# Performance work log

Measured on AMD Instinct MI355X. Metric: run time of the kernel, lower is better.

Reference implementation:

```python
import jax, jax.numpy as jnp
import numpy as np

# FIR kernel from resample_kernel=(1,3,3,1): outer product, normalized (gain=1)
_FIR_1D = np.array([1.0, 3.0, 3.0, 1.0], dtype=np.float32)
_FIR = np.outer(_FIR_1D, _FIR_1D)
_FIR = _FIR / _FIR.sum()  # 4x4


def setup_inputs() -> dict:
    key = jax.random.key(0)
    k1, k2, k3 = jax.random.split(key, 3)
    x = jax.random.normal(k1, (16, 256, 64, 64), dtype=jnp.float32)
    # fan_avg uniform init (default_init): variance = 1/fan_avg, fan_in=fan_out=256*9
    scale = float(np.sqrt(3.0 / (256 * 9)))
    w = jax.random.uniform(k2, (256, 256, 3, 3), dtype=jnp.float32, minval=-scale, maxval=scale)
    b = jax.random.normal(k3, (256,), dtype=jnp.float32) * 0.01
    return {"x": x, "w": w, "b": b}


def reference(x, w, b):
    # conv_downsample_2d: upfirdn2d(x, k, pad=(2,2)) then conv2d stride 2, then + bias
    B, C, H, W = x.shape
    # upfirdn2d with up=1, down=1 == zero-padded true convolution with k.
    # k is symmetric so flip is a no-op, but keep it for faithfulness.
    fir = jnp.asarray(_FIR[::-1, ::-1])                       # [4,4]
    fir_k = jnp.tile(fir[None, None, :, :], (C, 1, 1, 1))     # [C,1,4,4] depthwise
    x = jax.lax.conv_general_dilated(
        x, fir_k,
        window_strides=(1, 1),
        padding=((2, 2), (2, 2)),                             # (p+1)//2, p//2 with p=4
        feature_group_count=C,
        dimension_numbers=("NCHW", "OIHW", "NCHW"),
    )                                                          # [B,C,H+1,W+1]
    y = jax.lax.conv_general_dilated(
        x, w,
        window_strides=(2, 2),
        padding="VALID",
        dimension_numbers=("NCHW", "OIHW", "NCHW"),
    )                                                          # [B,outC,H//2,W//2]
    return y + b[None, :, None, None]
```

## Files before the change

### kernel.cpp

```cpp
#include <hip/hip_runtime.h>
#include <hip/hip_bf16.h>

typedef __attribute__((ext_vector_type(8))) short bf16x8;
typedef __attribute__((ext_vector_type(4))) float f32x4;
typedef __attribute__((ext_vector_type(8))) unsigned short u16x8;

#define KD 2304
#define OUT_PER_B (256 * 1024)

static __device__ __forceinline__ ushort f2bf(float f) {
  union { float f; unsigned int i; } v; v.f = f;
  unsigned int x = v.i;
  x += 0x7fffu + ((x >> 16) & 1u);
  return (ushort)(x >> 16);
}
static __device__ __forceinline__ float bf2f(ushort u) {
  union { unsigned int i; float f; } v; v.i = ((unsigned)u) << 16; return v.f;
}

#define GLDS16(gp, lp)                                                         \
  __builtin_amdgcn_global_load_lds(                                            \
      (const __attribute__((address_space(1))) void*)(gp),                     \
      (__attribute__((address_space(3))) void*)(lp), 16, 0, 0)

#define SWZ(g, r) (((g) & 8) | (((g) ^ (r)) & 7))

__global__ __launch_bounds__(256) void k_fir3(const float* __restrict__ x,
                                              ushort* __restrict__ xft,
                                              const float* __restrict__ wsrc,
                                              ushort* __restrict__ wb) {
  __shared__ float sx[32 * 84];
  __shared__ ushort ring[4 * 65 * 34];
  const int band = blockIdx.x;
  const int c0 = blockIdx.y * 32;
  const int b = blockIdx.z;
  const int r0 = band * 13;
  const int t = threadIdx.x;

  {
    int flat = band + 5 * (blockIdx.y + 8 * b);
    for (int iw = flat * 256 + t; iw < 589824; iw += 163840) {
      float v = wsrc[iw];
      int j = iw % 9;
      int t2 = iw / 9;
      int ic = t2 & 255, oc = t2 >> 8;
      wb[oc * KD + j * 256 + ic] = f2bf(v);
    }
  }

  if (t < 128) {
    int r = t >> 2, cs = t & 3;
    sx[r * 84 + (cs < 2 ? 2 + cs : 66 + cs)] = 0.f;
  }

  for (int it = 0; it < 17; ++it) {
    const int ir = r0 - 2 + it;

    float4 rg[2];
    if (it <= 15) {
      if (ir >= 0 && ir < 64) {
#pragma unroll
        for (int i = 0; i < 2; ++i) {
          int f4 = i * 256 + t;
          int c = f4 >> 4, q = f4 & 15;
          rg[i] = *(const float4*)(x +
                    ((size_t)((b * 256 + c0 + c) * 64 + ir) << 6) + q * 4);
        }
      } else {
        rg[0] = rg[1] = make_float4(0.f, 0.f, 0.f, 0.f);
      }
    }

    if (it >= 4) {
      const int o = r0 - 4 + it;
      for (int idx = t; idx < 260; idx += 256) {
        int w = idx >> 2, a = idx & 3;
        u16x8 r4[4];
#pragma unroll
        for (int d = 0; d < 4; ++d) {
          int slot = (o - 2 + d) & 3;
          r4[d] = *(const u16x8*)&ring[(slot * 65 + w) * 34 + a * 8];
        }
        u16x8 ov;
#pragma unroll
        for (int k = 0; k < 8; ++k) {
          float f0 = bf2f(r4[0][k]), f1 = bf2f(r4[1][k]);
          float f2 = bf2f(r4[2][k]), f3 = bf2f(r4[3][k]);
          ov[k] = f2bf(((f0 + f3) + 3.f * (f1 + f2)) * 0.015625f);
        }
        *(u16x8*)&xft[((size_t)(b * 4225 + o * 65 + w) << 8) + c0 + a * 8] = ov;
      }
    }

    if (it <= 15) {
#pragma unroll
      for (int i = 0; i < 2; ++i) {
        int f4 = i * 256 + t;
        int c = f4 >> 4, q = f4 & 15;
        *(float4*)&sx[c * 84 + 4 + q * 4] = rg[i];
      }
    }
    __syncthreads();

    if (it <= 15) {
      ushort* rw = ring + (ir & 3) * 65 * 34;
      for (int idx = t; idx < 544; idx += 256) {
        int g = idx >> 5, c = idx & 31;
        const float* s = &sx[c * 84 + g * 4];
        float4 a0 = *(const float4*)(s);
        float4 a1 = *(const float4*)(s + 4);
        float4 a2 = *(const float4*)(s + 8);
        int w0 = g * 4;
        rw[w0 * 34 + c] = f2bf((a0.z + a1.y) + 3.f * (a0.w + a1.x));
        if (w0 + 1 < 65) rw[(w0 + 1) * 34 + c] = f2bf((a0.w + a1.z) + 3.f * (a1.x + a1.y));
        if (w0 + 2 < 65) rw[(w0 + 2) * 34 + c] = f2bf((a1.x + a1.w) + 3.f * (a1.y + a1.z));
        if (w0 + 3 < 65) rw[(w0 + 3) * 34 + c] = f2bf((a1.y + a2.x) + 3.f * (a1.z + a1.w));
      }
    }
    __syncthreads();
  }
}

__global__ __launch_bounds__(256) void k_gemm3(const ushort* __restrict__ Wb,
                                               const ushort* __restrict__ Xt,
                                               const float* __restrict__ bias,
                                               float* __restrict__ out) {
  __shared__ ushort lA[128 * 128];
  __shared__ ushort lB[64 * 128];
  const int bid = blockIdx.x;
  const int work = (bid & 7) * 64 + (bid >> 3);
  const int ntile = work >> 1;
  const int mtile = work & 1;
  const int m0 = mtile * 128;
  const int n0 = ntile * 64;
  const int t = threadIdx.x;
  const int wid = t >> 6, lane = t & 63;
  const int wm = wid >> 1, wn = wid & 1;
  const int lrow = lane & 15, kgrp = lane >> 4;

  const ushort* aB[8];
#pragma unroll
  for (int i = 0; i < 8; ++i) {
    int idx = i * 256 + t;
    int row = idx >> 4, gL = idx & 15;
    aB[i] = Wb + (size_t)(m0 + row) * KD + SWZ(gL, row) * 8;
  }
  const ushort* bB[4];
#pragma unroll
  for (int i = 0; i < 4; ++i) {
    int idx = i * 256 + t;
    int row = idx >> 4, gL = idx & 15;
    int n = n0 + row;
    int b = n >> 10, oh = (n >> 5) & 31, ow = n & 31;
    bB[i] = Xt + ((size_t)((b * 65 + 2 * oh) * 65 + 2 * ow) << 8) +
            SWZ(gL, row) * 8;
  }

  f32x4 acc[4][2];
#pragma unroll
  for (int i = 0; i < 4; ++i)
#pragma unroll
    for (int j = 0; j < 2; ++j) acc[i][j] = (f32x4){0.f, 0.f, 0.f, 0.f};

  for (int kt = 0; kt < 18; ++kt) {
    const int j = kt >> 1;
    const int dh = j / 3, dw = j - 3 * dh;
    const int boff = (dh * 65 + dw) * 256 + ((kt & 1) << 7);
    const int k0 = kt << 7;
    __syncthreads();
#pragma unroll
    for (int i = 0; i < 8; ++i)
      GLDS16(aB[i] + k0, &lA[(i * 256 + t) * 8]);
#pragma unroll
    for (int i = 0; i < 4; ++i)
      GLDS16(bB[i] + boff, &lB[(i * 256 + t) * 8]);
    __syncthreads();

#pragma unroll
    for (int s = 0; s < 4; ++s) {
      bf16x8 Af[4], Bf[2];
#pragma unroll
      for (int f = 0; f < 4; ++f) {
        int row = wm * 64 + f * 16 + lrow;
        Af[f] = *(const bf16x8*)&lA[row * 128 + SWZ(s * 4 + kgrp, row) * 8];
      }
#pragma unroll
      for (int f = 0; f < 2; ++f) {
        int row = wn * 32 + f * 16 + lrow;
        Bf[f] = *(const bf16x8*)&lB[row * 128 + SWZ(s * 4 + kgrp, row) * 8];
      }
#pragma unroll
      for (int fm = 0; fm < 4; ++fm)
#pragma unroll
        for (int fn = 0; fn < 2; ++fn)
          acc[fm][fn] = __builtin_amdgcn_mfma_f32_16x16x32_bf16(
              Af[fm], Bf[fn], acc[fm][fn], 0, 0, 0);
    }
  }

  f32x4 bv[4];
#pragma unroll
  for (int fm = 0; fm < 4; ++fm)
    bv[fm] = *(const f32x4*)(bias + m0 + wm * 64 + fm * 16 + kgrp * 4);

#pragma unroll
  for (int fm = 0; fm < 4; ++fm) {
#pragma unroll
    for (int fn = 0; fn < 2; ++fn) {
      int nn = n0 + wn * 32 + fn * 16 + lrow;
      int oc = m0 + wm * 64 + fm * 16 + kgrp * 4;
      float* op = out + (size_t)(nn >> 10) * OUT_PER_B + (nn & 1023) +
                  (size_t)oc * 1024;
      op[0]    = acc[fm][fn][0] + bv[fm][0];
      op[1024] = acc[fm][fn][1] + bv[fm][1];
      op[2048] = acc[fm][fn][2] + bv[fm][2];
      op[3072] = acc[fm][fn][3] + bv[fm][3];
    }
  }
}

extern "C" void kernel_launch(void* const* d_in, const int* in_sizes, int n_in,
                              void* d_out, int out_size, void* d_ws, size_t ws_size,
                              hipStream_t stream) {
  const float* x    = (const float*)d_in[0];
  const float* w    = (const float*)d_in[1];
  const float* bias = (const float*)d_in[2];
  float* out = (float*)d_out;

  char* ws = (char*)d_ws;
  ushort* xft = (ushort*)ws;
  ushort* wb  = (ushort*)(ws + 34611200);

  k_fir3<<<dim3(5, 8, 16), 256, 0, stream>>>(x, xft, w, wb);
  k_gemm3<<<512, 256, 0, stream>>>(wb, xft, bias, out);
}
```

Baseline: 68.15 us.

## Split FIR block into independent per-wave channel groups with wave barriers

The FIR prepass now gives each of the four waves its own 8-channel slice with private LDS staging and ring buffers, replacing block-wide __syncthreads with wave-level barriers. This removes the cross-wave synchronization stalls in the 17-iteration row loop and lets waves progress independently. In exchange the vertical pass uses 65 of 64 lanes unevenly (one lane does two columns), and the xft writes become 16-byte chunks per wave rather than coalesced 64-byte groups. Correctness relies on wave-synchronous LDS visibility within a wavefront.

```diff
diff --git a/kernel.cpp b/kernel.cpp
--- a/kernel.cpp
+++ b/kernel.cpp
@@ -25,20 +25,24 @@
 
 #define SWZ(g, r) (((g) & 8) | (((g) ^ (r)) & 7))
 
-__global__ __launch_bounds__(256) void k_fir3(const float* __restrict__ x,
+__global__ __launch_bounds__(256) void k_fir4(const float* __restrict__ x,
                                               ushort* __restrict__ xft,
                                               const float* __restrict__ wsrc,
                                               ushort* __restrict__ wb) {
-  __shared__ float sx[32 * 84];
-  __shared__ ushort ring[4 * 65 * 34];
+  __shared__ float sxAll[4][8 * 84];
+  __shared__ ushort ringAll[4][4 * 65 * 8];
   const int band = blockIdx.x;
-  const int c0 = blockIdx.y * 32;
+  const int cg = blockIdx.y;
   const int b = blockIdx.z;
+  const int t = threadIdx.x;
+  const int wid = t >> 6, lane = t & 63;
+  const int coct = cg * 32 + wid * 8;
   const int r0 = band * 13;
-  const int t = threadIdx.x;
+  float* sx = sxAll[wid];
+  ushort* ring = ringAll[wid];
 
   {
-    int flat = band + 5 * (blockIdx.y + 8 * b);
+    int flat = band + 5 * (cg + 8 * b);
     for (int iw = flat * 256 + t; iw < 589824; iw += 163840) {
       float v = wsrc[iw];
       int j = iw % 9;
@@ -48,38 +52,36 @@
     }
   }
 
-  if (t < 128) {
-    int r = t >> 2, cs = t & 3;
+  if (lane < 32) {
+    int r = lane >> 2, cs = lane & 3;
     sx[r * 84 + (cs < 2 ? 2 + cs : 66 + cs)] = 0.f;
   }
 
   for (int it = 0; it < 17; ++it) {
     const int ir = r0 - 2 + it;
 
-    float4 rg[2];
+    float4 rg0, rg1;
     if (it <= 15) {
       if (ir >= 0 && ir < 64) {
-#pragma unroll
-        for (int i = 0; i < 2; ++i) {
-          int f4 = i * 256 + t;
-          int c = f4 >> 4, q = f4 & 15;
-          rg[i] = *(const float4*)(x +
-                    ((size_t)((b * 256 + c0 + c) * 64 + ir) << 6) + q * 4);
-        }
+        rg0 = *(const float4*)(x +
+              ((size_t)((b * 256 + coct + (lane >> 4)) * 64 + ir) << 6) +
+              (lane & 15) * 4);
+        rg1 = *(const float4*)(x +
+              ((size_t)((b * 256 + coct + 4 + (lane >> 4)) * 64 + ir) << 6) +
+              (lane & 15) * 4);
       } else {
-        rg[0] = rg[1] = make_float4(0.f, 0.f, 0.f, 0.f);
+        rg0 = rg1 = make_float4(0.f, 0.f, 0.f, 0.f);
       }
     }
 
     if (it >= 4) {
       const int o = r0 - 4 + it;
-      for (int idx = t; idx < 260; idx += 256) {
-        int w = idx >> 2, a = idx & 3;
+      for (int w = lane; w < 65; w += 64) {
         u16x8 r4[4];
 #pragma unroll
         for (int d = 0; d < 4; ++d) {
           int slot = (o - 2 + d) & 3;
-          r4[d] = *(const u16x8*)&ring[(slot * 65 + w) * 34 + a * 8];
+          r4[d] = *(const u16x8*)&ring[(slot * 65 + w) * 8];
         }
         u16x8 ov;
 #pragma unroll
@@ -88,36 +90,32 @@
           float f2 = bf2f(r4[2][k]), f3 = bf2f(r4[3][k]);
           ov[k] = f2bf(((f0 + f3) + 3.f * (f1 + f2)) * 0.015625f);
         }
-        *(u16x8*)&xft[((size_t)(b * 4225 + o * 65 + w) << 8) + c0 + a * 8] = ov;
+        *(u16x8*)&xft[((size_t)(b * 4225 + o * 65 + w) << 8) + coct] = ov;
       }
     }
 
     if (it <= 15) {
-#pragma unroll
-      for (int i = 0; i < 2; ++i) {
-        int f4 = i * 256 + t;
-        int c = f4 >> 4, q = f4 & 15;
-        *(float4*)&sx[c * 84 + 4 + q * 4] = rg[i];
-      }
-    }
-    __syncthreads();
+      *(float4*)&sx[(lane >> 4) * 84 + 4 + (lane & 15) * 4] = rg0;
+      *(float4*)&sx[(4 + (lane >> 4)) * 84 + 4 + (lane & 15) * 4] = rg1;
+    }
+    __builtin_amdgcn_wave_barrier();
 
     if (it <= 15) {
-      ushort* rw = ring + (ir & 3) * 65 * 34;
-      for (int idx = t; idx < 544; idx += 256) {
-        int g = idx >> 5, c = idx & 31;
+      ushort* rw = ring + (ir & 3) * 65 * 8;
+      for (int idx = lane; idx < 136; idx += 64) {
+        int g = idx >> 3, c = idx & 7;
         const float* s = &sx[c * 84 + g * 4];
         float4 a0 = *(const float4*)(s);
         float4 a1 = *(const float4*)(s + 4);
         float4 a2 = *(const float4*)(s + 8);
         int w0 = g * 4;
-        rw[w0 * 34 + c] = f2bf((a0.z + a1.y) + 3.f * (a0.w + a1.x));
-        if (w0 + 1 < 65) rw[(w0 + 1) * 34 + c] = f2bf((a0.w + a1.z) + 3.f * (a1.x + a1.y));
-        if (w0 + 2 < 65) rw[(w0 + 2) * 34 + c] = f2bf((a1.x + a1.w) + 3.f * (a1.y + a1.z));
-        if (w0 + 3 < 65) rw[(w0 + 3) * 34 + c] = f2bf((a1.y + a2.x) + 3.f * (a1.z + a1.w));
-      }
-    }
-    __syncthreads();
+        rw[w0 * 8 + c] = f2bf((a0.z + a1.y) + 3.f * (a0.w + a1.x));
+        if (w0 + 1 < 65) rw[(w0 + 1) * 8 + c] = f2bf((a0.w + a1.z) + 3.f * (a1.x + a1.y));
+        if (w0 + 2 < 65) rw[(w0 + 2) * 8 + c] = f2bf((a1.x + a1.w) + 3.f * (a1.y + a1.z));
+        if (w0 + 3 < 65) rw[(w0 + 3) * 8 + c] = f2bf((a1.y + a2.x) + 3.f * (a1.z + a1.w));
+      }
+    }
+    __builtin_amdgcn_wave_barrier();
   }
 }
 
@@ -231,6 +229,6 @@
   ushort* xft = (ushort*)ws;
   ushort* wb  = (ushort*)(ws + 34611200);
 
-  k_fir3<<<dim3(5, 8, 16), 256, 0, stream>>>(x, xft, w, wb);
+  k_fir4<<<dim3(5, 8, 16), 256, 0, stream>>>(x, xft, w, wb);
   k_gemm3<<<512, 256, 0, stream>>>(wb, xft, bias, out);
 }
```

Result: no change. 67.56 us (-0.9%).
